# Kernel tuning notes

Measured on AMD Instinct MI355X. Metric: run time of the kernel, lower is better.

The kernel has to match this reference:

```python
import jax, jax.numpy as jnp
import numpy as np

B, T, M, P, F = 1024, 50, 128, 128, 64  # batch, timesteps, enc_hidden, dec_hidden, feat
BN_EPS = 1e-5


def setup_inputs() -> dict:
    key = jax.random.key(0)
    ks = jax.random.split(key, 20)
    s = 0.05
    inp = {
        "X_encoded": jax.random.normal(ks[0], (B, T, M), jnp.float32),
        "y_prev": jax.random.normal(ks[1], (B, T, F), jnp.float32),
        # attn_layer: Linear(2P+M -> M), Tanh, Linear(M -> 1)
        "attn_w1": jax.random.normal(ks[2], (M, 2 * P + M), jnp.float32) * s,
        "attn_b1": jnp.zeros((M,), jnp.float32),
        "attn_w2": jax.random.normal(ks[3], (1, M), jnp.float32) * s,
        "attn_b2": jnp.zeros((1,), jnp.float32),
        # fc: Linear(M+F -> F) + BatchNorm1d(F) (eval mode, running stats)
        "fc_w": jax.random.normal(ks[4], (F, M + F), jnp.float32) * s,
        "fc_b": jnp.zeros((F,), jnp.float32),
        "bn_gamma": jnp.ones((F,), jnp.float32),
        "bn_beta": jnp.zeros((F,), jnp.float32),
        "bn_mean": jnp.zeros((F,), jnp.float32),
        "bn_var": jnp.ones((F,), jnp.float32),
        # 2-layer LSTM (input F -> hidden P); gate order i,f,g,o as in torch
        "w_ih0": jax.random.normal(ks[5], (4 * P, F), jnp.float32) * s,
        "w_hh0": jax.random.normal(ks[6], (4 * P, P), jnp.float32) * s,
        "b_ih0": jnp.zeros((4 * P,), jnp.float32),
        "b_hh0": jnp.zeros((4 * P,), jnp.float32),
        "w_ih1": jax.random.normal(ks[7], (4 * P, P), jnp.float32) * s,
        "w_hh1": jax.random.normal(ks[8], (4 * P, P), jnp.float32) * s,
        "b_ih1": jnp.zeros((4 * P,), jnp.float32),
        "b_hh1": jnp.zeros((4 * P,), jnp.float32),
        # fc_final: Linear(P+M -> F) + ReLU
        "fcf_w": jax.random.normal(ks[9], (F, P + M), jnp.float32) * s,
        "fcf_b": jnp.zeros((F,), jnp.float32),
    }
    return inp


def _lstm_cell(x, h, c, w_ih, w_hh, b_ih, b_hh):
    g = x @ w_ih.T + b_ih + h @ w_hh.T + b_hh
    i, f, gg, o = jnp.split(g, 4, axis=-1)
    c2 = jax.nn.sigmoid(f) * c + jax.nn.sigmoid(i) * jnp.tanh(gg)
    h2 = jax.nn.sigmoid(o) * jnp.tanh(c2)
    return h2, c2


def reference(X_encoded, y_prev, attn_w1, attn_b1, attn_w2, attn_b2,
              fc_w, fc_b, bn_gamma, bn_beta, bn_mean, bn_var,
              w_ih0, w_hh0, b_ih0, b_hh0, w_ih1, w_hh1, b_ih1, b_hh1,
              fcf_w, fcf_b):
    b, t, m = X_encoded.shape
    p = w_hh0.shape[1]
    # split attn W1 over the concat [d_n[-1]; c_n[-1]; X_encoded]
    w1_d = attn_w1[:, :p]
    w1_c = attn_w1[:, p:2 * p]
    w1_x = attn_w1[:, 2 * p:]
    x_proj = jnp.einsum('btm,nm->btn', X_encoded, w1_x)  # [B,T,M], loop-invariant

    def step(carry, y_t):
        h0, c0, h1, c1, _ = carry
        state_proj = h1 @ w1_d.T + c1 @ w1_c.T + attn_b1          # [B,M]
        score = jnp.tanh(x_proj + state_proj[:, None, :]) @ attn_w2[0] + attn_b2[0]  # [B,T]
        beta = jax.nn.softmax(score, axis=1)
        context = jnp.einsum('bt,btm->bm', beta, X_encoded)        # [B,M]
        z = jnp.concatenate([context, y_t], axis=1) @ fc_w.T + fc_b
        y_tilde = (z - bn_mean) * jax.lax.rsqrt(bn_var + BN_EPS) * bn_gamma + bn_beta
        h0n, c0n = _lstm_cell(y_tilde, h0, c0, w_ih0, w_hh0, b_ih0, b_hh0)
        h1n, c1n = _lstm_cell(h0n, h1, c1, w_ih1, w_hh1, b_ih1, b_hh1)
        return (h0n, c0n, h1n, c1n, context), None

    zeros_p = jnp.zeros((b, p), X_encoded.dtype)
    zeros_m = jnp.zeros((b, m), X_encoded.dtype)
    init = (zeros_p, zeros_p, zeros_p, zeros_p, zeros_m)
    (h0, c0, h1, c1, context), _ = jax.lax.scan(init=init, f=step, xs=jnp.swapaxes(y_prev, 0, 1))
    y_pred = jax.nn.relu(jnp.concatenate([h1, context], axis=1) @ fcf_w.T + fcf_b)
    return y_pred
```

## Files before the change

kernel.cpp:

```cpp
#include <hip/hip_runtime.h>
#include <math.h>

#define TT 50
#define MM 128
#define PP 128
#define FF 64
#define NB 4
#define NTHR 512
#define BN_EPS 1e-5f

typedef unsigned int   u32;
typedef unsigned short u16;
typedef _Float16 f16x8 __attribute__((ext_vector_type(8)));
typedef float    f32x4 __attribute__((ext_vector_type(4)));

#define MFMA16(a, b, c) __builtin_amdgcn_mfma_f32_16x16x32_f16((a), (b), (c), 0, 0, 0)

__device__ __forceinline__ float fsig(float x)  { return 1.0f / (1.0f + __expf(-x)); }
__device__ __forceinline__ float ftanh(float x) { return 1.0f - 2.0f / (__expf(2.0f * x) + 1.0f); }
__device__ __forceinline__ u16 f2h(float x) { _Float16 h = (_Float16)x; u16 r; __builtin_memcpy(&r, &h, 2); return r; }
__device__ __forceinline__ float h2f(u16 u) { _Float16 h; __builtin_memcpy(&h, &u, 2); return (float)h; }

__device__ __forceinline__ void lds_barrier() {
    asm volatile("s_waitcnt lgkmcnt(0)\n\ts_barrier" ::: "memory");
}

__global__ __launch_bounds__(256) void packA_k(const float* __restrict__ w1, u16* __restrict__ dst) {
    int i = blockIdx.x * 256 + threadIdx.x;
    if (i >= 8 * 8 * 64 * 8) return;
    int j = i & 7, l = (i >> 3) & 63, ks = (i >> 9) & 7, tile = i >> 12;
    int row = tile * 16 + (l & 15);
    int k = ks * 32 + ((l >> 4) & 3) * 8 + j;
    dst[i] = f2h(w1[row * 384 + k]);
}
__global__ __launch_bounds__(256) void packE_k(const float* __restrict__ fcw, u16* __restrict__ dst) {
    int i = blockIdx.x * 256 + threadIdx.x;
    if (i >= 4 * 6 * 64 * 8) return;
    int j = i & 7, l = (i >> 3) & 63, r = i >> 9;
    int ks = r % 6, tile = r / 6;
    int row = tile * 16 + (l & 15);
    int k = ks * 32 + ((l >> 4) & 3) * 8 + j;
    dst[i] = f2h(fcw[row * 192 + k]);
}
__global__ __launch_bounds__(256) void packF_k(const float* __restrict__ wih0, const float* __restrict__ whh0,
                                               u16* __restrict__ dst) {
    int i = blockIdx.x * 256 + threadIdx.x;
    if (i >= 8 * 24 * 64 * 8) return;
    int j = i & 7, l = (i >> 3) & 63, rem = i >> 9;
    int wv = rem / 24, t = rem % 24, ks = t >> 2, g = t & 3;
    int row = g * 128 + wv * 16 + (l & 15);
    int k = ks * 32 + ((l >> 4) & 3) * 8 + j;
    float v = (k < 64) ? wih0[row * 64 + k] : whh0[row * 128 + (k - 64)];
    dst[i] = f2h(v);
}
__global__ __launch_bounds__(256) void packG_k(const float* __restrict__ wih1, const float* __restrict__ whh1,
                                               u16* __restrict__ dst) {
    int i = blockIdx.x * 256 + threadIdx.x;
    if (i >= 8 * 32 * 64 * 8) return;
    int j = i & 7, l = (i >> 3) & 63, rem = i >> 9;
    int wv = rem >> 5, t = rem & 31, ks = t >> 2, g = t & 3;
    int row = g * 128 + wv * 16 + (l & 15);
    int k = ks * 32 + ((l >> 4) & 3) * 8 + j;
    float v = (k < 128) ? wih1[row * 128 + k] : whh1[row * 128 + (k - 128)];
    dst[i] = f2h(v);
}

__global__ __launch_bounds__(NTHR, 2) void decoder_kernel(
    const float* __restrict__ X,
    const float* __restrict__ yprev,
    const float* __restrict__ w1,
    const float* __restrict__ b1,
    const float* __restrict__ w2,
    const float* __restrict__ b2,
    const float* __restrict__ fcb,
    const float* __restrict__ bng,
    const float* __restrict__ bnb,
    const float* __restrict__ bnm,
    const float* __restrict__ bnv,
    const float* __restrict__ bih0,
    const float* __restrict__ bhh0,
    const float* __restrict__ bih1,
    const float* __restrict__ bhh1,
    const float* __restrict__ fcfw,
    const float* __restrict__ fcfb,
    const u16* __restrict__ pA,
    const u16* __restrict__ pE,
    const u16* __restrict__ pF,
    const u16* __restrict__ pG,
    float* __restrict__ out)
{
    __shared__ __align__(16) u16   Xh[NB][TT][136];
    __shared__ __align__(16) u16   xph[NB][TT][140];
    __shared__ __align__(16) u16   h0h[2][NB][144];
    __shared__ __align__(16) u16   h1h[2][NB][144];
    __shared__ __align__(16) u16   c1h[NB][144];
    __shared__ __align__(16) u16   ytilh[NB][72];
    __shared__ __align__(16) u16   ctyh[NB][200];
    __shared__ __align__(16) float spf[NB][132];
    __shared__ __align__(16) float c0f[NB][132], c1f[NB][132];
    __shared__ __align__(16) float scs[NB][68];
    __shared__ __align__(16) float b1s[128], w2s[128];
    __shared__ __align__(16) float fck0s[FF], fck1s[FF];
    __shared__ __align__(16) float bsum0s[512], bsum1s[512];

    const int tid = threadIdx.x;
    const int b0 = blockIdx.x * NB;
    const int wv = tid >> 6, l = tid & 63;
    const int kg = (l >> 4) & 3;
    const int c4 = l & 3;
    const int cown = l & 15;

    for (int i4 = tid; i4 < NB * TT * 32; i4 += NTHR) {
        int bb = i4 / (TT * 32);
        int r  = i4 % (TT * 32);
        float4 v = ((const float4*)(X + (size_t)(b0 + bb) * TT * MM))[r];
        uint2 pk;
        pk.x = (u32)f2h(v.x) | ((u32)f2h(v.y) << 16);
        pk.y = (u32)f2h(v.z) | ((u32)f2h(v.w) << 16);
        *(uint2*)&Xh[bb][r >> 5][(r & 31) * 4] = pk;
    }
    for (int i = tid; i < NB * 144; i += NTHR) {
        int bb = i / 144, k = i % 144;
        h0h[0][bb][k] = 0; h0h[1][bb][k] = 0;
        h1h[0][bb][k] = 0; h1h[1][bb][k] = 0;
        c1h[bb][k] = 0;
        if (k < 132) { c0f[bb][k] = 0.f; c1f[bb][k] = 0.f; }
    }
    if (tid < 128) { b1s[tid] = b1[tid]; w2s[tid] = w2[tid]; }
    else if (tid < 192) {
        int f = tid - 128;
        float k1 = rsqrtf(bnv[f] + BN_EPS) * bng[f];
        fck1s[f] = k1;
        fck0s[f] = (fcb[f] - bnm[f]) * k1 + bnb[f];
    }
    bsum0s[tid] = bih0[tid] + bhh0[tid];
    bsum1s[tid] = bih1[tid] + bhh1[tid];

    const int bq = tid >> 7, rr = tid & 127;
    const bool own = rr < 2 * TT;
    const int tq = rr >> 1, qq = rr & 1;
    const float b2v = b2[0];

    if (own) {
        float xf[64];
        #pragma unroll
        for (int n = 0; n < 64; ++n) xf[n] = 0.f;
        const float* Xrow = X + ((size_t)(b0 + bq) * TT + tq) * MM;
        for (int m4 = 0; m4 < 32; ++m4) {
            float4 xv = *(const float4*)(Xrow + m4 * 4);
            #pragma unroll
            for (int n = 0; n < 64; ++n) {
                float4 w = *(const float4*)(w1 + (size_t)(qq * 64 + n) * 384 + 256 + m4 * 4);
                xf[n] += xv.x * w.x + xv.y * w.y + xv.z * w.z + xv.w * w.w;
            }
        }
        #pragma unroll
        for (int j = 0; j < 32; ++j) {
            u32 pk = (u32)f2h(xf[2 * j]) | ((u32)f2h(xf[2 * j + 1]) << 16);
            *(u32*)&xph[bq][tq][qq * 64 + 2 * j] = pk;
        }
    }
    __syncthreads();

    for (int ts = 0; ts < TT; ++ts) {
        const int p = ts & 1;

        {
            f32x4 acc = *(const f32x4*)&b1s[wv * 16 + kg * 4];
            const u16* abase = pA + (size_t)(wv * 8) * 512 + (size_t)l * 8;
            #pragma unroll
            for (int ks = 0; ks < 8; ++ks) {
                f16x8 a = *(const f16x8*)(abase + ks * 512);
                const u16* bp = (ks < 4) ? &h1h[p][c4][ks * 32 + kg * 8]
                                         : &c1h[c4][(ks - 4) * 32 + kg * 8];
                acc = MFMA16(a, *(const f16x8*)bp, acc);
            }
            if (cown < 4) *(f32x4*)&spf[cown][wv * 16 + kg * 4] = acc;
        }
        f16x8 ew[6];
        if (wv < 4) {
            const u16* abase = pE + (size_t)(wv * 6) * 512 + (size_t)l * 8;
            #pragma unroll
            for (int ks = 0; ks < 6; ++ks) ew[ks] = *(const f16x8*)(abase + ks * 512);
        }
        lds_barrier();

        if (own) {
            float acc = 0.f;
            #pragma unroll
            for (int jb = 0; jb < 8; ++jb) {
                uint4 xv = *(const uint4*)&xph[bq][tq][qq * 64 + jb * 8];
                int n = qq * 64 + jb * 8;
                acc += ftanh(h2f((u16)(xv.x & 0xffffu)) + spf[bq][n + 0]) * w2s[n + 0];
                acc += ftanh(h2f((u16)(xv.x >> 16))     + spf[bq][n + 1]) * w2s[n + 1];
                acc += ftanh(h2f((u16)(xv.y & 0xffffu)) + spf[bq][n + 2]) * w2s[n + 2];
                acc += ftanh(h2f((u16)(xv.y >> 16))     + spf[bq][n + 3]) * w2s[n + 3];
                acc += ftanh(h2f((u16)(xv.z & 0xffffu)) + spf[bq][n + 4]) * w2s[n + 4];
                acc += ftanh(h2f((u16)(xv.z >> 16))     + spf[bq][n + 5]) * w2s[n + 5];
                acc += ftanh(h2f((u16)(xv.w & 0xffffu)) + spf[bq][n + 6]) * w2s[n + 6];
                acc += ftanh(h2f((u16)(xv.w >> 16))     + spf[bq][n + 7]) * w2s[n + 7];
            }
            acc += __shfl_xor(acc, 1);
            if (qq == 0) scs[bq][tq] = acc + b2v;
        }
        lds_barrier();

        if (tid < 256) {
            int b = tid >> 6, t = tid & 63;
            float v = (t < TT) ? scs[b][t] : -1e30f;
            float mx = v;
            #pragma unroll
            for (int o = 32; o; o >>= 1) mx = fmaxf(mx, __shfl_xor(mx, o));
            float e = (t < TT) ? __expf(v - mx) : 0.f;
            float s = e;
            #pragma unroll
            for (int o = 32; o; o >>= 1) s += __shfl_xor(s, o);
            if (t < TT) scs[b][t] = e / s;
        } else {
            int i = tid - 256; int bb = i >> 6, f = i & 63;
            ctyh[bb][128 + f] = f2h(yprev[((size_t)(b0 + bb) * TT + ts) * FF + f]);
        }
        lds_barrier();

        f16x8 fw0[8];
        {
            const u16* pw = pF + (size_t)wv * 24 * 512 + (size_t)l * 8;
            #pragma unroll
            for (int q = 0; q < 8; ++q) fw0[q] = *(const f16x8*)(pw + q * 512);
        }
        {
            int bb = tid >> 7, m = tid & 127;
            float acc = 0.f;
            #pragma unroll 10
            for (int t = 0; t < TT; ++t) acc += scs[bb][t] * h2f(Xh[bb][t][m]);
            ctyh[bb][m] = f2h(acc);
        }
        lds_barrier();

        if (wv < 4) {
            f32x4 acc = {0.f, 0.f, 0.f, 0.f};
            #pragma unroll
            for (int ks = 0; ks < 6; ++ks) {
                f16x8 b = *(const f16x8*)&ctyh[c4][ks * 32 + kg * 8];
                acc = MFMA16(ew[ks], b, acc);
            }
            if (cown < 4) {
                int row = wv * 16 + kg * 4;
                f32x4 k1 = *(const f32x4*)&fck1s[row];
                f32x4 k0 = *(const f32x4*)&fck0s[row];
                #pragma unroll
                for (int r = 0; r < 4; ++r)
                    ytilh[cown][row + r] = f2h(acc[r] * k1[r] + k0[r]);
            }
        }
        lds_barrier();

        {
            const u16* pw = pF + (size_t)wv * 24 * 512 + (size_t)l * 8;
            f32x4 a0 = *(const f32x4*)&bsum0s[0 * 128 + wv * 16 + kg * 4];
            f32x4 a1 = *(const f32x4*)&bsum0s[1 * 128 + wv * 16 + kg * 4];
            f32x4 a2 = *(const f32x4*)&bsum0s[2 * 128 + wv * 16 + kg * 4];
            f32x4 a3 = *(const f32x4*)&bsum0s[3 * 128 + wv * 16 + kg * 4];
            #pragma unroll
            for (int ks = 0; ks < 2; ++ks) {
                f16x8 b = *(const f16x8*)&ytilh[c4][ks * 32 + kg * 8];
                a0 = MFMA16(fw0[ks * 4 + 0], b, a0);
                a1 = MFMA16(fw0[ks * 4 + 1], b, a1);
                a2 = MFMA16(fw0[ks * 4 + 2], b, a2);
                a3 = MFMA16(fw0[ks * 4 + 3], b, a3);
            }
            #pragma unroll
            for (int ks = 2; ks < 6; ++ks) {
                f16x8 b = *(const f16x8*)&h0h[p][c4][(ks - 2) * 32 + kg * 8];
                a0 = MFMA16(*(const f16x8*)(pw + (ks * 4 + 0) * 512), b, a0);
                a1 = MFMA16(*(const f16x8*)(pw + (ks * 4 + 1) * 512), b, a1);
                a2 = MFMA16(*(const f16x8*)(pw + (ks * 4 + 2) * 512), b, a2);
                a3 = MFMA16(*(const f16x8*)(pw + (ks * 4 + 3) * 512), b, a3);
            }
            if (cown < 4) {
                int cb = wv * 16 + kg * 4;
                u32 lo, hi;
                {
                    float gi = fsig(a0[0]), gF = fsig(a1[0]), gG = ftanh(a2[0]), gO = fsig(a3[0]);
                    float cn = gF * c0f[cown][cb + 0] + gi * gG;
                    c0f[cown][cb + 0] = cn;
                    lo = (u32)f2h(gO * ftanh(cn));
                }
                {
                    float gi = fsig(a0[1]), gF = fsig(a1[1]), gG = ftanh(a2[1]), gO = fsig(a3[1]);
                    float cn = gF * c0f[cown][cb + 1] + gi * gG;
                    c0f[cown][cb + 1] = cn;
                    lo |= (u32)f2h(gO * ftanh(cn)) << 16;
                }
                {
                    float gi = fsig(a0[2]), gF = fsig(a1[2]), gG = ftanh(a2[2]), gO = fsig(a3[2]);
                    float cn = gF * c0f[cown][cb + 2] + gi * gG;
                    c0f[cown][cb + 2] = cn;
                    hi = (u32)f2h(gO * ftanh(cn));
                }
                {
                    float gi = fsig(a0[3]), gF = fsig(a1[3]), gG = ftanh(a2[3]), gO = fsig(a3[3]);
                    float cn = gF * c0f[cown][cb + 3] + gi * gG;
                    c0f[cown][cb + 3] = cn;
                    hi |= (u32)f2h(gO * ftanh(cn)) << 16;
                }
                uint2 pk; pk.x = lo; pk.y = hi;
                *(uint2*)&h0h[p ^ 1][cown][cb] = pk;
            }
        }
        lds_barrier();

        {
            const u16* pw = pG + (size_t)wv * 32 * 512 + (size_t)l * 8;
            f32x4 a0 = *(const f32x4*)&bsum1s[0 * 128 + wv * 16 + kg * 4];
            f32x4 a1 = *(const f32x4*)&bsum1s[1 * 128 + wv * 16 + kg * 4];
            f32x4 a2 = *(const f32x4*)&bsum1s[2 * 128 + wv * 16 + kg * 4];
            f32x4 a3 = *(const f32x4*)&bsum1s[3 * 128 + wv * 16 + kg * 4];
            #pragma unroll
            for (int ks = 0; ks < 8; ++ks) {
                const u16* bp = (ks < 4) ? &h0h[p ^ 1][c4][ks * 32 + kg * 8]
                                         : &h1h[p][c4][(ks - 4) * 32 + kg * 8];
                f16x8 b = *(const f16x8*)bp;
                a0 = MFMA16(*(const f16x8*)(pw + (ks * 4 + 0) * 512), b, a0);
                a1 = MFMA16(*(const f16x8*)(pw + (ks * 4 + 1) * 512), b, a1);
                a2 = MFMA16(*(const f16x8*)(pw + (ks * 4 + 2) * 512), b, a2);
                a3 = MFMA16(*(const f16x8*)(pw + (ks * 4 + 3) * 512), b, a3);
            }
            if (cown < 4) {
                int cb = wv * 16 + kg * 4;
                u32 lo, hi;
                u32 clo, chi;
                {
                    float gi = fsig(a0[0]), gF = fsig(a1[0]), gG = ftanh(a2[0]), gO = fsig(a3[0]);
                    float cn = gF * c1f[cown][cb + 0] + gi * gG;
                    c1f[cown][cb + 0] = cn;
                    clo = (u32)f2h(cn);
                    lo  = (u32)f2h(gO * ftanh(cn));
                }
                {
                    float gi = fsig(a0[1]), gF = fsig(a1[1]), gG = ftanh(a2[1]), gO = fsig(a3[1]);
                    float cn = gF * c1f[cown][cb + 1] + gi * gG;
                    c1f[cown][cb + 1] = cn;
                    clo |= (u32)f2h(cn) << 16;
                    lo  |= (u32)f2h(gO * ftanh(cn)) << 16;
                }
                {
                    float gi = fsig(a0[2]), gF = fsig(a1[2]), gG = ftanh(a2[2]), gO = fsig(a3[2]);
                    float cn = gF * c1f[cown][cb + 2] + gi * gG;
                    c1f[cown][cb + 2] = cn;
                    chi = (u32)f2h(cn);
                    hi  = (u32)f2h(gO * ftanh(cn));
                }
                {
                    float gi = fsig(a0[3]), gF = fsig(a1[3]), gG = ftanh(a2[3]), gO = fsig(a3[3]);
                    float cn = gF * c1f[cown][cb + 3] + gi * gG;
                    c1f[cown][cb + 3] = cn;
                    chi |= (u32)f2h(cn) << 16;
                    hi  |= (u32)f2h(gO * ftanh(cn)) << 16;
                }
                uint2 pk; pk.x = lo; pk.y = hi;
                *(uint2*)&h1h[p ^ 1][cown][cb] = pk;
                uint2 ck; ck.x = clo; ck.y = chi;
                *(uint2*)&c1h[cown][cb] = ck;
            }
        }
        lds_barrier();
    }

    if (tid < 256) {
        int f = tid >> 2, bb = tid & 3;
        const float* wr = fcfw + (size_t)f * 256;
        float acc = fcfb[f];
        #pragma unroll 4
        for (int k4 = 0; k4 < 32; ++k4) {
            float4 w = *(const float4*)(wr + k4 * 4);
            acc += w.x * h2f(h1h[0][bb][k4 * 4 + 0]) + w.y * h2f(h1h[0][bb][k4 * 4 + 1])
                 + w.z * h2f(h1h[0][bb][k4 * 4 + 2]) + w.w * h2f(h1h[0][bb][k4 * 4 + 3]);
        }
        #pragma unroll 4
        for (int k4 = 0; k4 < 32; ++k4) {
            float4 w = *(const float4*)(wr + 128 + k4 * 4);
            acc += w.x * h2f(ctyh[bb][k4 * 4 + 0]) + w.y * h2f(ctyh[bb][k4 * 4 + 1])
                 + w.z * h2f(ctyh[bb][k4 * 4 + 2]) + w.w * h2f(ctyh[bb][k4 * 4 + 3]);
        }
        out[(size_t)(b0 + bb) * FF + f] = fmaxf(acc, 0.f);
    }
}

extern "C" void kernel_launch(void* const* d_in, const int* in_sizes, int n_in,
                              void* d_out, int out_size, void* d_ws, size_t ws_size,
                              hipStream_t stream) {
    (void)in_sizes; (void)n_in; (void)out_size; (void)ws_size;
    const float* X    = (const float*)d_in[0];
    const float* yp   = (const float*)d_in[1];
    const float* w1   = (const float*)d_in[2];
    const float* b1   = (const float*)d_in[3];
    const float* w2   = (const float*)d_in[4];
    const float* b2   = (const float*)d_in[5];
    const float* fcw  = (const float*)d_in[6];
    const float* fcb  = (const float*)d_in[7];
    const float* bng  = (const float*)d_in[8];
    const float* bnb  = (const float*)d_in[9];
    const float* bnm  = (const float*)d_in[10];
    const float* bnv  = (const float*)d_in[11];
    const float* wih0 = (const float*)d_in[12];
    const float* whh0 = (const float*)d_in[13];
    const float* bih0 = (const float*)d_in[14];
    const float* bhh0 = (const float*)d_in[15];
    const float* wih1 = (const float*)d_in[16];
    const float* whh1 = (const float*)d_in[17];
    const float* bih1 = (const float*)d_in[18];
    const float* bhh1 = (const float*)d_in[19];
    const float* fcfw = (const float*)d_in[20];
    const float* fcfb = (const float*)d_in[21];
    float* out = (float*)d_out;

    u16* pA = (u16*)d_ws;
    u16* pE = pA + 32768;
    u16* pF = pE + 12288;
    u16* pG = pF + 98304;

    packA_k<<<dim3(32768 / 256), dim3(256), 0, stream>>>(w1, pA);
    packE_k<<<dim3(12288 / 256), dim3(256), 0, stream>>>(fcw, pE);
    packF_k<<<dim3(98304 / 256), dim3(256), 0, stream>>>(wih0, whh0, pF);
    packG_k<<<dim3(131072 / 256), dim3(256), 0, stream>>>(wih1, whh1, pG);

    decoder_kernel<<<dim3(1024 / NB), dim3(NTHR), 0, stream>>>(
        X, yp, w1, b1, w2, b2, fcb, bng, bnb, bnm, bnv,
        bih0, bhh0, bih1, bhh1, fcfw, fcfb, pA, pE, pF, pG, out);
}
```

Baseline: 863.7 us.

## Halve batch rows per block and split attention work across more threads

After: 1.380 ms. 1.6x slower.

```diff
diff --git a/kernel.cpp b/kernel.cpp
--- a/kernel.cpp
+++ b/kernel.cpp
@@ -5,7 +5,7 @@
 #define MM 128
 #define PP 128
 #define FF 64
-#define NB 4
+#define NB 2
 #define NTHR 512
 #define BN_EPS 1e-5f
 
@@ -107,7 +107,7 @@
     const int b0 = blockIdx.x * NB;
     const int wv = tid >> 6, l = tid & 63;
     const int kg = (l >> 4) & 3;
-    const int c4 = l & 3;
+    const int c4 = l & 1;
     const int cown = l & 15;
 
     for (int i4 = tid; i4 < NB * TT * 32; i4 += NTHR) {
@@ -119,8 +119,8 @@
         pk.y = (u32)f2h(v.z) | ((u32)f2h(v.w) << 16);
         *(uint2*)&Xh[bb][r >> 5][(r & 31) * 4] = pk;
     }
-    for (int i = tid; i < NB * 144; i += NTHR) {
-        int bb = i / 144, k = i % 144;
+    if (tid < NB * 144) {
+        int bb = tid / 144, k = tid % 144;
         h0h[0][bb][k] = 0; h0h[1][bb][k] = 0;
         h1h[0][bb][k] = 0; h1h[1][bb][k] = 0;
         c1h[bb][k] = 0;
@@ -136,28 +136,28 @@
     bsum0s[tid] = bih0[tid] + bhh0[tid];
     bsum1s[tid] = bih1[tid] + bhh1[tid];
 
-    const int bq = tid >> 7, rr = tid & 127;
-    const bool own = rr < 2 * TT;
-    const int tq = rr >> 1, qq = rr & 1;
+    const int bq = tid >> 8, rr = tid & 255;
+    const bool own = rr < 4 * TT;
+    const int tq = rr >> 2, qq = rr & 3;
     const float b2v = b2[0];
 
     if (own) {
-        float xf[64];
+        float xf[32];
         #pragma unroll
-        for (int n = 0; n < 64; ++n) xf[n] = 0.f;
+        for (int n = 0; n < 32; ++n) xf[n] = 0.f;
         const float* Xrow = X + ((size_t)(b0 + bq) * TT + tq) * MM;
         for (int m4 = 0; m4 < 32; ++m4) {
             float4 xv = *(const float4*)(Xrow + m4 * 4);
             #pragma unroll
-            for (int n = 0; n < 64; ++n) {
-                float4 w = *(const float4*)(w1 + (size_t)(qq * 64 + n) * 384 + 256 + m4 * 4);
+            for (int n = 0; n < 32; ++n) {
+                float4 w = *(const float4*)(w1 + (size_t)(qq * 32 + n) * 384 + 256 + m4 * 4);
                 xf[n] += xv.x * w.x + xv.y * w.y + xv.z * w.z + xv.w * w.w;
             }
         }
         #pragma unroll
-        for (int j = 0; j < 32; ++j) {
+        for (int j = 0; j < 16; ++j) {
             u32 pk = (u32)f2h(xf[2 * j]) | ((u32)f2h(xf[2 * j + 1]) << 16);
-            *(u32*)&xph[bq][tq][qq * 64 + 2 * j] = pk;
+            *(u32*)&xph[bq][tq][qq * 32 + 2 * j] = pk;
         }
     }
     __syncthreads();
@@ -175,7 +175,7 @@
                                          : &c1h[c4][(ks - 4) * 32 + kg * 8];
                 acc = MFMA16(a, *(const f16x8*)bp, acc);
             }
-            if (cown < 4) *(f32x4*)&spf[cown][wv * 16 + kg * 4] = acc;
+            if (cown < NB) *(f32x4*)&spf[cown][wv * 16 + kg * 4] = acc;
         }
         f16x8 ew[6];
         if (wv < 4) {
@@ -188,9 +188,9 @@
         if (own) {
             float acc = 0.f;
             #pragma unroll
-            for (int jb = 0; jb < 8; ++jb) {
-                uint4 xv = *(const uint4*)&xph[bq][tq][qq * 64 + jb * 8];
-                int n = qq * 64 + jb * 8;
+            for (int jb = 0; jb < 4; ++jb) {
+                uint4 xv = *(const uint4*)&xph[bq][tq][qq * 32 + jb * 8];
+                int n = qq * 32 + jb * 8;
                 acc += ftanh(h2f((u16)(xv.x & 0xffffu)) + spf[bq][n + 0]) * w2s[n + 0];
                 acc += ftanh(h2f((u16)(xv.x >> 16))     + spf[bq][n + 1]) * w2s[n + 1];
                 acc += ftanh(h2f((u16)(xv.y & 0xffffu)) + spf[bq][n + 2]) * w2s[n + 2];
@@ -201,11 +201,12 @@
                 acc += ftanh(h2f((u16)(xv.w >> 16))     + spf[bq][n + 7]) * w2s[n + 7];
             }
             acc += __shfl_xor(acc, 1);
+            acc += __shfl_xor(acc, 2);
             if (qq == 0) scs[bq][tq] = acc + b2v;
         }
         lds_barrier();
 
-        if (tid < 256) {
+        if (tid < 128) {
             int b = tid >> 6, t = tid & 63;
             float v = (t < TT) ? scs[b][t] : -1e30f;
             float mx = v;
@@ -216,8 +217,8 @@
             #pragma unroll
             for (int o = 32; o; o >>= 1) s += __shfl_xor(s, o);
             if (t < TT) scs[b][t] = e / s;
-        } else {
-            int i = tid - 256; int bb = i >> 6, f = i & 63;
+        } else if (tid < 256) {
+            int i = tid - 128; int bb = i >> 6, f = i & 63;
             ctyh[bb][128 + f] = f2h(yprev[((size_t)(b0 + bb) * TT + ts) * FF + f]);
         }
         lds_barrier();
@@ -229,11 +230,15 @@
             for (int q = 0; q < 8; ++q) fw0[q] = *(const f16x8*)(pw + q * 512);
         }
         {
-            int bb = tid >> 7, m = tid & 127;
+            int bb = tid >> 8, m = (tid >> 1) & 127, thD = tid & 1;
             float acc = 0.f;
-            #pragma unroll 10
-            for (int t = 0; t < TT; ++t) acc += scs[bb][t] * h2f(Xh[bb][t][m]);
-            ctyh[bb][m] = f2h(acc);
+            #pragma unroll
+            for (int t = 0; t < 25; ++t) {
+                int tt = thD * 25 + t;
+                acc += scs[bb][tt] * h2f(Xh[bb][tt][m]);
+            }
+            acc += __shfl_xor(acc, 1);
+            if (thD == 0) ctyh[bb][m] = f2h(acc);
         }
         lds_barrier();
 
@@ -244,7 +249,7 @@
                 f16x8 b = *(const f16x8*)&ctyh[c4][ks * 32 + kg * 8];
                 acc = MFMA16(ew[ks], b, acc);
             }
-            if (cown < 4) {
+            if (cown < NB) {
                 int row = wv * 16 + kg * 4;
                 f32x4 k1 = *(const f32x4*)&fck1s[row];
                 f32x4 k0 = *(const f32x4*)&fck0s[row];
@@ -277,7 +282,7 @@
                 a2 = MFMA16(*(const f16x8*)(pw + (ks * 4 + 2) * 512), b, a2);
                 a3 = MFMA16(*(const f16x8*)(pw + (ks * 4 + 3) * 512), b, a3);
             }
-            if (cown < 4) {
+            if (cown < NB) {
                 int cb = wv * 16 + kg * 4;
                 u32 lo, hi;
                 {
@@ -326,10 +331,9 @@
                 a2 = MFMA16(*(const f16x8*)(pw + (ks * 4 + 2) * 512), b, a2);
                 a3 = MFMA16(*(const f16x8*)(pw + (ks * 4 + 3) * 512), b, a3);
             }
-            if (cown < 4) {
+            if (cown < NB) {
                 int cb = wv * 16 + kg * 4;
-                u32 lo, hi;
-                u32 clo, chi;
+                u32 lo, hi, clo, chi;
                 {
                     float gi = fsig(a0[0]), gF = fsig(a1[0]), gG = ftanh(a2[0]), gO = fsig(a3[0]);
                     float cn = gF * c1f[cown][cb + 0] + gi * gG;
@@ -367,8 +371,8 @@
         lds_barrier();
     }
 
-    if (tid < 256) {
-        int f = tid >> 2, bb = tid & 3;
+    if (tid < 128) {
+        int f = tid >> 1, bb = tid & 1;
         const float* wr = fcfw + (size_t)f * 256;
         float acc = fcfb[f];
         #pragma unroll 4
```
